# Kernel optimization log

Measured on AMD Instinct MI355X. Metric: run time of the kernel, lower is better.

## Reference

```python
import jax, jax.numpy as jnp
import numpy as np

N_NODES = 100000
N_EDGES = 1600000
D_IN = 128
D_OUT = 128


def setup_inputs() -> dict:
    key = jax.random.key(0)
    ks = jax.random.split(key, 8)
    h = jax.random.normal(ks[0], (N_NODES, D_IN), dtype=jnp.float32)
    edge_val = jax.random.uniform(ks[1], (N_EDGES,), dtype=jnp.float32)
    # Linear weights in torch layout [out, in]
    W_self = jax.random.normal(ks[2], (D_OUT, D_IN), dtype=jnp.float32) * (1.0 / np.sqrt(D_IN))
    b_self = jax.random.normal(ks[3], (D_OUT,), dtype=jnp.float32) * 0.01
    W_nb = jax.random.normal(ks[4], (D_OUT, D_IN), dtype=jnp.float32) * (1.0 / np.sqrt(D_IN))
    b_nb = jax.random.normal(ks[5], (D_OUT,), dtype=jnp.float32) * 0.01
    edge_row = jax.random.randint(ks[6], (N_EDGES,), 0, N_NODES, dtype=jnp.int64)
    edge_col = jax.random.randint(ks[7], (N_EDGES,), 0, N_NODES, dtype=jnp.int64)
    return {"h": h, "edge_val": edge_val, "W_self": W_self, "b_self": b_self,
            "W_nb": W_nb, "b_nb": b_nb, "edge_row": edge_row, "edge_col": edge_col}


def reference(h, edge_val, W_self, b_self, W_nb, b_nb, edge_row, edge_col):
    # self_h = Linear_self(h[:out_nodes]); out_nodes == N_NODES here
    self_h = h @ W_self.T + b_self  # [N, D_OUT]
    # neighbor_h = adj.spmm(h): sparse COO (row, col, val) times dense h
    msgs = edge_val[:, None] * h[edge_col]            # [E, D_IN]
    neighbor_h = jax.ops.segment_sum(msgs, edge_row, num_segments=N_NODES)  # [N, D_IN]
    out = self_h + neighbor_h @ W_nb.T + b_nb
    return out
```

## Files before the change

kernel.cpp:

```cpp
#include <hip/hip_runtime.h>


constexpr int NN = 100000;
constexpr int NE = 1600000;
constexpr int D  = 128;
constexpr int NBUCK  = 500;
constexpr int BROWS  = 200;
constexpr int BCAP   = 3584;
constexpr int CHUNK  = 2048;
constexpr int NCH    = (NE + CHUNK - 1) / CHUNK;
constexpr int GM     = 64;
constexpr int TPB    = 2;
constexpr int NGB    = (NN + GM * TPB - 1) / (GM * TPB);
constexpr int LP     = 132;

typedef __bf16 bf16x8 __attribute__((ext_vector_type(8)));
typedef float  f32x4  __attribute__((ext_vector_type(4)));
typedef float  f32x2  __attribute__((ext_vector_type(2)));
typedef unsigned short u16x4 __attribute__((ext_vector_type(4)));

__global__ __launch_bounds__(256) void gemm_mfma(
    const float* __restrict__ h,
    const float* __restrict__ Wself,
    const float* __restrict__ Wnb,
    const float* __restrict__ bself,
    const float* __restrict__ bnb,
    float* __restrict__ out,
    __bf16* __restrict__ tmpb)
{
    __shared__ __bf16 hs[2][GM * LP];
    const int t    = threadIdx.x;
    const int w    = t >> 6;
    const int lane = t & 63;
    const int l15  = lane & 15;
    const int quad = lane >> 4;
    const int base_row = blockIdx.x * GM * TPB;

    bf16x8 wf[4][4];
    #pragma unroll
    for (int ns = 0; ns < 4; ++ns) {
        int wrow = w * 64 + ns * 16 + l15;
        const float* wr = (wrow < D) ? (Wself + (size_t)wrow * D)
                                     : (Wnb + (size_t)(wrow - D) * D);
        #pragma unroll
        for (int kk = 0; kk < 4; ++kk) {
            f32x4 lo = *(const f32x4*)(wr + kk * 32 + quad * 8);
            f32x4 hi = *(const f32x4*)(wr + kk * 32 + quad * 8 + 4);
            bf16x8 bb;
            #pragma unroll
            for (int j = 0; j < 4; ++j) { bb[j] = (__bf16)lo[j]; bb[4 + j] = (__bf16)hi[j]; }
            wf[ns][kk] = bb;
        }
    }
    f32x4 biasv[4];
    #pragma unroll
    for (int ns = 0; ns < 4; ++ns) {
        int col = w * 64 + ns * 16 + quad * 4;
        if (col < D) {
            f32x4 b1 = *(const f32x4*)(bself + col);
            f32x4 b2 = *(const f32x4*)(bnb + col);
            biasv[ns] = b1 + b2;
        } else biasv[ns] = (f32x4){0.f, 0.f, 0.f, 0.f};
    }

    {
        #pragma unroll
        for (int it = 0; it < 4; ++it) {
            int idx = it * 2048 + t * 8;
            int r = idx >> 7, c = idx & 127;
            int gr = base_row + r; if (gr >= NN) gr = NN - 1;
            f32x4 lo = *(const f32x4*)(h + (size_t)gr * D + c);
            f32x4 hi = *(const f32x4*)(h + (size_t)gr * D + c + 4);
            bf16x8 v;
            #pragma unroll
            for (int j = 0; j < 4; ++j) { v[j] = (__bf16)lo[j]; v[4 + j] = (__bf16)hi[j]; }
            *(bf16x8*)(&hs[0][r * LP + c]) = v;
        }
    }
    __syncthreads();

    #pragma unroll
    for (int tt = 0; tt < TPB; ++tt) {
        const int row0 = base_row + tt * GM;

        f32x4 pf[8];
        if (tt + 1 < TPB) {
            #pragma unroll
            for (int it = 0; it < 4; ++it) {
                int idx = it * 2048 + t * 8;
                int r = idx >> 7, c = idx & 127;
                int gr = base_row + GM + r; if (gr >= NN) gr = NN - 1;
                pf[it * 2]     = *(const f32x4*)(h + (size_t)gr * D + c);
                pf[it * 2 + 1] = *(const f32x4*)(h + (size_t)gr * D + c + 4);
            }
        }

        f32x4 acc[4][4];
        #pragma unroll
        for (int mi = 0; mi < 4; ++mi)
            #pragma unroll
            for (int ns = 0; ns < 4; ++ns) acc[mi][ns] = (f32x4){0.f, 0.f, 0.f, 0.f};

        #pragma unroll
        for (int mi = 0; mi < 4; ++mi) {
            bf16x8 hf[4];
            #pragma unroll
            for (int kk = 0; kk < 4; ++kk)
                hf[kk] = *(const bf16x8*)(&hs[tt & 1][(mi * 16 + l15) * LP + quad * 8 + kk * 32]);
            #pragma unroll
            for (int ns = 0; ns < 4; ++ns)
                #pragma unroll
                for (int kk = 0; kk < 4; ++kk)
                    acc[mi][ns] = __builtin_amdgcn_mfma_f32_16x16x32_bf16(wf[ns][kk], hf[kk], acc[mi][ns], 0, 0, 0);
        }

        if (tt + 1 < TPB) {
            #pragma unroll
            for (int it = 0; it < 4; ++it) {
                int idx = it * 2048 + t * 8;
                int r = idx >> 7, c = idx & 127;
                bf16x8 v;
                #pragma unroll
                for (int j = 0; j < 4; ++j) {
                    v[j]     = (__bf16)pf[it * 2][j];
                    v[4 + j] = (__bf16)pf[it * 2 + 1][j];
                }
                *(bf16x8*)(&hs[(tt + 1) & 1][r * LP + c]) = v;
            }
            __syncthreads();
        }

        #pragma unroll
        for (int mi = 0; mi < 4; ++mi) {
            int row = row0 + mi * 16 + l15;
            if (row < NN) {
                if (w < 2) {
                    #pragma unroll
                    for (int ns = 0; ns < 4; ++ns) {
                        int col = w * 64 + ns * 16 + quad * 4;
                        *(f32x4*)(out + (size_t)row * D + col) = acc[mi][ns] + biasv[ns];
                    }
                } else {
                    #pragma unroll
                    for (int ns = 0; ns < 4; ++ns) {
                        int col = (w - 2) * 64 + ns * 16 + quad * 4;
                        u16x4 v;
                        #pragma unroll
                        for (int i = 0; i < 4; ++i) {
                            __bf16 b = (__bf16)acc[mi][ns][i];
                            v[i] = *(unsigned short*)&b;
                        }
                        *(u16x4*)(tmpb + (size_t)row * D + col) = v;
                    }
                }
            }
        }
    }
}

__global__ __launch_bounds__(256) void wc_scatter(
    const int* __restrict__ erow, const int* __restrict__ ecol,
    const float* __restrict__ eval_,
    int* __restrict__ gcount, int2* __restrict__ epair)
{
    __shared__ int  cnt[NBUCK];
    __shared__ int  lscan[NBUCK];
    __shared__ int  gbase[NBUCK];
    __shared__ int  ss[512];
    __shared__ int2 sbuf[CHUNK];
    __shared__ int  saddr[CHUNK];
    __shared__ int  s_total;

    const int t  = threadIdx.x;
    const int c0 = blockIdx.x * CHUNK;

    for (int b = t; b < NBUCK; b += 256) cnt[b] = 0;
    __syncthreads();

    int   bp[8];
    int   colr[8];
    float valr[8];
    #pragma unroll
    for (int j = 0; j < 8; ++j) {
        int e = c0 + j * 256 + t;
        if (e < NE) {
            int r   = erow[e];
            colr[j] = ecol[e];
            valr[j] = eval_[e];
            int b   = r / BROWS;
            int rlo = r - b * BROWS;
            int pos = atomicAdd(&cnt[b], 1);
            bp[j]   = b | (rlo << 9) | (pos << 17);
        } else bp[j] = -1;
    }
    __syncthreads();

    ss[t]       = (t < NBUCK)       ? cnt[t]       : 0;
    ss[t + 256] = (t + 256 < NBUCK) ? cnt[t + 256] : 0;
    __syncthreads();
    for (int off = 1; off < 512; off <<= 1) {
        int i0 = t, i1 = t + 256;
        int r0 = ss[i0] + ((i0 >= off) ? ss[i0 - off] : 0);
        int r1 = ss[i1] + ((i1 >= off) ? ss[i1 - off] : 0);
        __syncthreads();
        ss[i0] = r0; ss[i1] = r1;
        __syncthreads();
    }
    if (t < NBUCK) {
        int n = cnt[t];
        lscan[t] = ss[t] - n;
        gbase[t] = (n > 0) ? atomicAdd(&gcount[t], n) : 0;
    }
    if (t + 256 < NBUCK) {
        int n = cnt[t + 256];
        lscan[t + 256] = ss[t + 256] - n;
        gbase[t + 256] = (n > 0) ? atomicAdd(&gcount[t + 256], n) : 0;
    }
    if (t == 0) s_total = ss[511];
    __syncthreads();

    #pragma unroll
    for (int j = 0; j < 8; ++j) {
        if (bp[j] >= 0) {
            int b   = bp[j] & 511;
            int rlo = (bp[j] >> 9) & 255;
            int pos = bp[j] >> 17;
            int slot = lscan[b] + pos;
            sbuf[slot]  = make_int2(colr[j] | (rlo << 17), __float_as_int(valr[j]));
            saddr[slot] = b * BCAP + gbase[b] + pos;
        }
    }
    __syncthreads();

    int ce = s_total;
    for (int i = t; i < ce; i += 256)
        epair[saddr[i]] = sbuf[i];
}

__global__ __launch_bounds__(512) void bucket_sort(
    const int2* __restrict__ epair, const int* __restrict__ gcount,
    int2* __restrict__ epair2, int2* __restrict__ rowrange)
{
    __shared__ int  cnt[BROWS];
    __shared__ int  off2[BROWS];
    __shared__ int  cur[BROWS];
    __shared__ int  ss[256];
    __shared__ int2 sorted[BCAP];

    const int t = threadIdx.x;
    const int b = blockIdx.x;
    const int n = gcount[b];
    const int2* src = epair + (size_t)b * BCAP;

    if (t < BROWS) cnt[t] = 0;
    __syncthreads();

    int2 r[8];
    int  nr = 0;
    for (int i = t; i < n; i += 512) {
        int2 p = src[i];
        r[nr++] = p;
        atomicAdd(&cnt[(p.x >> 17) & 255], 1);
    }
    __syncthreads();

    if (t < 256) ss[t] = (t < BROWS) ? cnt[t] : 0;
    __syncthreads();
    for (int o = 1; o < 256; o <<= 1) {
        int y = 0;
        if (t < 256 && t >= o) y = ss[t - o];
        __syncthreads();
        if (t < 256) ss[t] += y;
        __syncthreads();
    }
    if (t < BROWS) {
        int v = cnt[t];
        off2[t] = ss[t] - v;
        cur[t]  = ss[t] - v;
    }
    __syncthreads();

    for (int j = 0; j < nr; ++j) {
        int slot = atomicAdd(&cur[(r[j].x >> 17) & 255], 1);
        sorted[slot] = r[j];
    }
    __syncthreads();

    const int base = b * BCAP;
    for (int i = t; i < n; i += 512)
        epair2[base + i] = sorted[i];
    if (t < BROWS) {
        int row = b * BROWS + t;
        if (row < NN)
            rowrange[row] = make_int2(base + off2[t], base + off2[t] + cnt[t]);
    }
}

__global__ __launch_bounds__(256) void aggregate(
    const __bf16* __restrict__ tmpb, const int2* __restrict__ rowrange,
    const int2* __restrict__ epair2, float* __restrict__ out,
    int row0, int nrows)
{
    int wave = row0 + ((blockIdx.x * 256 + threadIdx.x) >> 6);
    if (wave >= row0 + nrows) return;
    int lane = threadIdx.x & 63;
    int2 rr = rowrange[wave];
    int beg = __builtin_amdgcn_readfirstlane(rr.x);
    int end = __builtin_amdgcn_readfirstlane(rr.y);

    float ax[4] = {0.f, 0.f, 0.f, 0.f};
    float ay[4] = {0.f, 0.f, 0.f, 0.f};
    int e = beg;
    for (; e + 3 < end; e += 4) {
        int2 p[4];
        #pragma unroll
        for (int k = 0; k < 4; ++k) p[k] = epair2[e + k];
        #pragma unroll
        for (int k = 0; k < 4; ++k) {
            int col = p[k].x & 0x1FFFF;
            unsigned u = *(const unsigned*)(tmpb + (size_t)col * D + lane * 2);
            float v = __int_as_float(p[k].y);
            ax[k] += v * __uint_as_float(u << 16);
            ay[k] += v * __uint_as_float(u & 0xffff0000u);
        }
    }
    for (; e < end; ++e) {
        int2 p = epair2[e];
        int col = p.x & 0x1FFFF;
        unsigned u = *(const unsigned*)(tmpb + (size_t)col * D + lane * 2);
        float v = __int_as_float(p.y);
        ax[0] += v * __uint_as_float(u << 16);
        ay[0] += v * __uint_as_float(u & 0xffff0000u);
    }
    f32x2* o = (f32x2*)(out + (size_t)wave * D + lane * 2);
    f32x2 c = __builtin_nontemporal_load(o);
    c.x += (ax[0] + ax[1]) + (ax[2] + ax[3]);
    c.y += (ay[0] + ay[1]) + (ay[2] + ay[3]);
    __builtin_nontemporal_store(c, o);
}

extern "C" void kernel_launch(void* const* d_in, const int* in_sizes, int n_in,
                              void* d_out, int out_size, void* d_ws, size_t ws_size,
                              hipStream_t stream) {
    const float* h     = (const float*)d_in[0];
    const float* eval_ = (const float*)d_in[1];
    const float* Wself = (const float*)d_in[2];
    const float* bself = (const float*)d_in[3];
    const float* Wnb   = (const float*)d_in[4];
    const float* bnb   = (const float*)d_in[5];
    const int*   erow  = (const int*)d_in[6];
    const int*   ecol  = (const int*)d_in[7];
    float* out = (float*)d_out;

    char* p = (char*)d_ws;
    __bf16* tmpb    = (__bf16*)p;   p += (size_t)(NGB * GM * TPB) * D * 2;
    int2*   epair   = (int2*)p;     p += (size_t)NBUCK * BCAP * 8;
    int2*   epair2  = (int2*)p;     p += (size_t)NBUCK * BCAP * 8;
    int2*   rowrange= (int2*)p;     p += (size_t)NN * 8;
    int*    gcount  = (int*)p;

    hipMemsetAsync(gcount, 0, NBUCK * 4, stream);

    gemm_mfma<<<NGB, 256, 0, stream>>>(h, Wself, Wnb, bself, bnb, out, tmpb);
    wc_scatter<<<NCH, 256, 0, stream>>>(erow, ecol, eval_, gcount, epair);
    bucket_sort<<<NBUCK, 512, 0, stream>>>(epair, gcount, epair2, rowrange);
    aggregate<<<(50000 * 64) / 256, 256, 0, stream>>>(tmpb, rowrange, epair2, out, 0, 50000);
    aggregate<<<(50000 * 64) / 256, 256, 0, stream>>>(tmpb, rowrange, epair2, out, 50000, 50000);
}
```

Before: 263.1 us.

## Make GEMM persistent with double-buffered tiles, unroll aggregate by 8, merge launches

The GEMM kernel becomes persistent: a fixed grid of 512 blocks strides over 64-row tiles and prefetches the next tile into a double-buffered shared array. This amortises the per-block weight-fragment load and keeps the global loads for the next tile overlapped with MFMA work. The aggregate kernel gains an 8-edge unrolled loop to keep more gathers in flight, and its two half-size launches are merged into one. The trade-offs are higher register pressure from the 8-deep unroll, and the GEMM now relies on the fixed grid of 512 blocks spreading the tiles evenly across the GPU.

```diff
diff --git a/kernel.cpp b/kernel.cpp
--- a/kernel.cpp
+++ b/kernel.cpp
@@ -10,8 +10,8 @@
 constexpr int CHUNK  = 2048;
 constexpr int NCH    = (NE + CHUNK - 1) / CHUNK;
 constexpr int GM     = 64;
-constexpr int TPB    = 2;
-constexpr int NGB    = (NN + GM * TPB - 1) / (GM * TPB);
+constexpr int NT     = (NN + GM - 1) / GM;
+constexpr int GRID   = 512;
 constexpr int LP     = 132;
 
 typedef __bf16 bf16x8 __attribute__((ext_vector_type(8)));
@@ -34,7 +34,6 @@
     const int lane = t & 63;
     const int l15  = lane & 15;
     const int quad = lane >> 4;
-    const int base_row = blockIdx.x * GM * TPB;
 
     bf16x8 wf[4][4];
     #pragma unroll
@@ -63,35 +62,42 @@
         } else biasv[ns] = (f32x4){0.f, 0.f, 0.f, 0.f};
     }
 
+    int srow[4], scol[4];
+    #pragma unroll
+    for (int it = 0; it < 4; ++it) {
+        int idx = it * 2048 + t * 8;
+        srow[it] = idx >> 7;
+        scol[it] = idx & 127;
+    }
+
     {
+        const int row0 = blockIdx.x * GM;
         #pragma unroll
         for (int it = 0; it < 4; ++it) {
-            int idx = it * 2048 + t * 8;
-            int r = idx >> 7, c = idx & 127;
-            int gr = base_row + r; if (gr >= NN) gr = NN - 1;
-            f32x4 lo = *(const f32x4*)(h + (size_t)gr * D + c);
-            f32x4 hi = *(const f32x4*)(h + (size_t)gr * D + c + 4);
+            int gr = row0 + srow[it]; if (gr >= NN) gr = NN - 1;
+            f32x4 lo = *(const f32x4*)(h + (size_t)gr * D + scol[it]);
+            f32x4 hi = *(const f32x4*)(h + (size_t)gr * D + scol[it] + 4);
             bf16x8 v;
             #pragma unroll
             for (int j = 0; j < 4; ++j) { v[j] = (__bf16)lo[j]; v[4 + j] = (__bf16)hi[j]; }
-            *(bf16x8*)(&hs[0][r * LP + c]) = v;
-        }
-    }
-    __syncthreads();
-
-    #pragma unroll
-    for (int tt = 0; tt < TPB; ++tt) {
-        const int row0 = base_row + tt * GM;
+            *(bf16x8*)(&hs[0][srow[it] * LP + scol[it]]) = v;
+        }
+    }
+    __syncthreads();
+
+    int buf = 0;
+    for (int tile = blockIdx.x; tile < NT; tile += GRID) {
+        const int row0 = tile * GM;
+        const bool hasn = (tile + GRID) < NT;
 
         f32x4 pf[8];
-        if (tt + 1 < TPB) {
+        if (hasn) {
+            const int nrow0 = (tile + GRID) * GM;
             #pragma unroll
             for (int it = 0; it < 4; ++it) {
-                int idx = it * 2048 + t * 8;
-                int r = idx >> 7, c = idx & 127;
-                int gr = base_row + GM + r; if (gr >= NN) gr = NN - 1;
-                pf[it * 2]     = *(const f32x4*)(h + (size_t)gr * D + c);
-                pf[it * 2 + 1] = *(const f32x4*)(h + (size_t)gr * D + c + 4);
+                int gr = nrow0 + srow[it]; if (gr >= NN) gr = NN - 1;
+                pf[it * 2]     = *(const f32x4*)(h + (size_t)gr * D + scol[it]);
+                pf[it * 2 + 1] = *(const f32x4*)(h + (size_t)gr * D + scol[it] + 4);
             }
         }
 
@@ -101,12 +107,13 @@
             #pragma unroll
             for (int ns = 0; ns < 4; ++ns) acc[mi][ns] = (f32x4){0.f, 0.f, 0.f, 0.f};
 
+        const __bf16* hb = hs[buf];
         #pragma unroll
         for (int mi = 0; mi < 4; ++mi) {
             bf16x8 hf[4];
             #pragma unroll
             for (int kk = 0; kk < 4; ++kk)
-                hf[kk] = *(const bf16x8*)(&hs[tt & 1][(mi * 16 + l15) * LP + quad * 8 + kk * 32]);
+                hf[kk] = *(const bf16x8*)(&hb[(mi * 16 + l15) * LP + quad * 8 + kk * 32]);
             #pragma unroll
             for (int ns = 0; ns < 4; ++ns)
                 #pragma unroll
@@ -114,21 +121,19 @@
                     acc[mi][ns] = __builtin_amdgcn_mfma_f32_16x16x32_bf16(wf[ns][kk], hf[kk], acc[mi][ns], 0, 0, 0);
         }
 
-        if (tt + 1 < TPB) {
+        if (hasn) {
             #pragma unroll
             for (int it = 0; it < 4; ++it) {
-                int idx = it * 2048 + t * 8;
-                int r = idx >> 7, c = idx & 127;
                 bf16x8 v;
                 #pragma unroll
                 for (int j = 0; j < 4; ++j) {
                     v[j]     = (__bf16)pf[it * 2][j];
                     v[4 + j] = (__bf16)pf[it * 2 + 1][j];
                 }
-                *(bf16x8*)(&hs[(tt + 1) & 1][r * LP + c]) = v;
+                *(bf16x8*)(&hs[buf ^ 1][srow[it] * LP + scol[it]]) = v;
             }
-            __syncthreads();
-        }
+        }
+        __syncthreads();
 
         #pragma unroll
         for (int mi = 0; mi < 4; ++mi) {
@@ -155,6 +160,7 @@
                 }
             }
         }
+        buf ^= 1;
     }
 }
 
@@ -311,6 +317,19 @@
     float ax[4] = {0.f, 0.f, 0.f, 0.f};
     float ay[4] = {0.f, 0.f, 0.f, 0.f};
     int e = beg;
+    for (; e + 7 < end; e += 8) {
+        int2 p[8];
+        #pragma unroll
+        for (int k = 0; k < 8; ++k) p[k] = epair2[e + k];
+        #pragma unroll
+        for (int k = 0; k < 8; ++k) {
+            int col = p[k].x & 0x1FFFF;
+            unsigned u = *(const unsigned*)(tmpb + (size_t)col * D + lane * 2);
+            float v = __int_as_float(p[k].y);
+            ax[k & 3] += v * __uint_as_float(u << 16);
+            ay[k & 3] += v * __uint_as_float(u & 0xffff0000u);
+        }
+    }
     for (; e + 3 < end; e += 4) {
         int2 p[4];
         #pragma unroll
@@ -353,7 +372,7 @@
     float* out = (float*)d_out;
 
     char* p = (char*)d_ws;
-    __bf16* tmpb    = (__bf16*)p;   p += (size_t)(NGB * GM * TPB) * D * 2;
+    __bf16* tmpb    = (__bf16*)p;   p += (size_t)NT * GM * D * 2;
     int2*   epair   = (int2*)p;     p += (size_t)NBUCK * BCAP * 8;
     int2*   epair2  = (int2*)p;     p += (size_t)NBUCK * BCAP * 8;
     int2*   rowrange= (int2*)p;     p += (size_t)NN * 8;
@@ -361,9 +380,8 @@
 
     hipMemsetAsync(gcount, 0, NBUCK * 4, stream);
 
-    gemm_mfma<<<NGB, 256, 0, stream>>>(h, Wself, Wnb, bself, bnb, out, tmpb);
+    gemm_mfma<<<GRID, 256, 0, stream>>>(h, Wself, Wnb, bself, bnb, out, tmpb);
     wc_scatter<<<NCH, 256, 0, stream>>>(erow, ecol, eval_, gcount, epair);
     bucket_sort<<<NBUCK, 512, 0, stream>>>(epair, gcount, epair2, rowrange);
-    aggregate<<<(50000 * 64) / 256, 256, 0, stream>>>(tmpb, rowrange, epair2, out, 0, 50000);
-    aggregate<<<(50000 * 64) / 256, 256, 0, stream>>>(tmpb, rowrange, epair2, out, 50000, 50000);
-}
+    aggregate<<<(NN * 64) / 256, 256, 0, stream>>>(tmpb, rowrange, epair2, out, 0, NN);
+}
```

Result: faster. 251.8 us (-4.3%).
